# Kernel tuning notes

Hardware: AMD Instinct MI355X
Metric: run time of the kernel (lower is better)

The kernel has to match this reference:

```python
import jax, jax.numpy as jnp
import numpy as np

B, S, H = 4, 2048, 1024
NH, NKV, HD = 16, 4, 64
EPS = 1e-6
SCALE = 1.0 / np.sqrt(HD)
N_REP = NH // NKV


def setup_inputs() -> dict:
    key = jax.random.key(0)
    ks = jax.random.split(key, 8)
    hidden_states = jax.random.normal(ks[0], (B, S, H), dtype=jnp.float32)
    # additive causal mask [1,1,S,S]: 0 on/below diagonal, -1e9 above
    causal_mask = jnp.where(
        jnp.tril(jnp.ones((S, S), dtype=bool)), 0.0, -1e9
    ).astype(jnp.float32)[None, None]
    # interleaved RoPE tables [S, HD] (each frequency repeated twice, matching _rotate_half's even/odd split)
    inv_freq = 1.0 / (10000.0 ** (np.arange(0, HD, 2, dtype=np.float32) / HD))
    angles = jnp.arange(S, dtype=jnp.float32)[:, None] * jnp.asarray(inv_freq)[None, :]
    emb = jnp.repeat(angles, 2, axis=-1)  # [S, HD]
    cos, sin = jnp.cos(emb), jnp.sin(emb)
    # learned params (stored [in, out] for einsum)
    Wq = jax.random.normal(ks[1], (H, NH * HD), dtype=jnp.float32) * 0.02
    Wk = jax.random.normal(ks[2], (H, NKV * HD), dtype=jnp.float32) * 0.02
    Wv = jax.random.normal(ks[3], (H, NKV * HD), dtype=jnp.float32) * 0.02
    Wo = jax.random.normal(ks[4], (NH * HD, H), dtype=jnp.float32) * 0.02
    q_norm_w = jnp.ones((HD,), dtype=jnp.float32)
    k_norm_w = jnp.ones((HD,), dtype=jnp.float32)
    return {"hidden_states": hidden_states, "causal_mask": causal_mask, "cos": cos,
            "sin": sin, "Wq": Wq, "Wk": Wk, "Wv": Wv, "Wo": Wo,
            "q_norm_w": q_norm_w, "k_norm_w": k_norm_w}


def _rms_norm(x, w):
    var = jnp.mean(jnp.square(x), axis=-1, keepdims=True)
    return x * jax.lax.rsqrt(var + EPS) * w


def _rotate_half(x):
    x1 = x[..., ::2]
    x2 = x[..., 1::2]
    return jnp.stack((-x2, x1), axis=-1).reshape(x.shape)


def reference(hidden_states, causal_mask, cos, sin, Wq, Wk, Wv, Wo, q_norm_w, k_norm_w):
    b, s, _ = hidden_states.shape
    q = jnp.einsum('bsh,hd->bsd', hidden_states, Wq).reshape(b, s, NH, HD)
    k = jnp.einsum('bsh,hd->bsd', hidden_states, Wk).reshape(b, s, NKV, HD)
    v = jnp.einsum('bsh,hd->bsd', hidden_states, Wv).reshape(b, s, NKV, HD)
    q = _rms_norm(q, q_norm_w)
    k = _rms_norm(k, k_norm_w)
    q = q.transpose(0, 2, 1, 3)  # [b, NH, s, HD]
    k = k.transpose(0, 2, 1, 3)  # [b, NKV, s, HD]
    v = v.transpose(0, 2, 1, 3)
    c = cos[None, None]  # [1,1,s,HD]
    sn = sin[None, None]
    q = q * c + _rotate_half(q) * sn
    k = k * c + _rotate_half(k) * sn
    if N_REP > 1:
        k = jnp.repeat(k, N_REP, axis=1)  # GQA expand -> [b, NH, s, HD]
        v = jnp.repeat(v, N_REP, axis=1)
    scores = jnp.einsum('bhqd,bhkd->bhqk', q, k) * SCALE + causal_mask
    probs = jax.nn.softmax(scores, axis=-1)
    attn = jnp.einsum('bhqk,bhkd->bhqd', probs, v)
    attn = attn.transpose(0, 2, 1, 3).reshape(b, s, NH * HD)
    return jnp.einsum('bsd,dh->bsh', attn, Wo)
```

## Files before the change

kernel.cpp:

```cpp
#include <hip/hip_runtime.h>

typedef unsigned short u16;
typedef unsigned int u32;

typedef __attribute__((ext_vector_type(8))) short bf16x8;
typedef __attribute__((ext_vector_type(4))) float f32x4;

#define QSCALE 0.18033688011112042f

__device__ __forceinline__ u16 f2bf(float x) {
    union { float f; u32 u; } v; v.f = x;
    u32 r = (v.u + 0x7FFFu + ((v.u >> 16) & 1u)) >> 16;
    return (u16)r;
}
__device__ __forceinline__ float bf2f(u16 x) {
    union { u32 u; float f; } v; v.u = ((u32)x) << 16;
    return v.f;
}
__device__ __forceinline__ u32 pk2(float x, float y) {
    u32 ax = __float_as_uint(x) + 0x8000u;
    u32 ay = __float_as_uint(y) + 0x8000u;
    return __builtin_amdgcn_perm(ay, ax, 0x07060302u);
}

__device__ __forceinline__ void cp16(const u16* g, u16* l) {
    __builtin_amdgcn_global_load_lds(
        (__attribute__((address_space(1))) void*)(g),
        (__attribute__((address_space(3))) void*)(l), 16, 0, 0);
}

__global__ void k_prep(const float* __restrict__ hidden, u16* __restrict__ hA,
                       const float* __restrict__ Wq, u16* __restrict__ WqT,
                       const float* __restrict__ Wk, u16* __restrict__ WkT,
                       const float* __restrict__ Wv, u16* __restrict__ WvT,
                       const float* __restrict__ Wo, u16* __restrict__ WoT) {
    __shared__ u16 t[64][72];
    int bid = blockIdx.x, tid = threadIdx.x;
    if (bid < 4096) {
        int i = (bid * 256 + tid) * 8;
        float4 a = *(const float4*)(hidden + i);
        float4 b = *(const float4*)(hidden + i + 4);
        ushort4 o0; o0.x = f2bf(a.x); o0.y = f2bf(a.y); o0.z = f2bf(a.z); o0.w = f2bf(a.w);
        ushort4 o1; o1.x = f2bf(b.x); o1.y = f2bf(b.y); o1.z = f2bf(b.z); o1.w = f2bf(b.w);
        *(ushort4*)(hA + i) = o0;
        *(ushort4*)(hA + i + 4) = o1;
        return;
    }
    int rb = bid - 4096;
    const float* W; u16* Wt; int N, bx, by;
    if (rb < 256)      { W = Wq; Wt = WqT; N = 1024; bx = rb & 15; by = rb >> 4; }
    else if (rb < 320) { W = Wk; Wt = WkT; N = 256;  rb -= 256; bx = rb & 3; by = rb >> 2; }
    else if (rb < 384) { W = Wv; Wt = WvT; N = 256;  rb -= 320; bx = rb & 3; by = rb >> 2; }
    else               { W = Wo; Wt = WoT; N = 1024; rb -= 384; bx = rb & 15; by = rb >> 4; }
    const int K = 1024;
    int rr = tid >> 2;
    int cs = tid & 3;
    const float* src = W + (by*64 + rr)*N + bx*64 + cs*16;
#pragma unroll
    for (int j = 0; j < 16; j += 4) {
        float4 v = *(const float4*)(src + j);
        t[rr][cs*16 + j + 0] = f2bf(v.x);
        t[rr][cs*16 + j + 1] = f2bf(v.y);
        t[rr][cs*16 + j + 2] = f2bf(v.z);
        t[rr][cs*16 + j + 3] = f2bf(v.w);
    }
    __syncthreads();
    u16* dst = Wt + (bx*64 + rr)*K + by*64 + cs*16;
#pragma unroll
    for (int j = 0; j < 16; ++j) dst[j] = t[cs*16 + j][rr];
}

__device__ __forceinline__ void stage_ab(const u16* __restrict__ Asrc, const u16* __restrict__ Bsrc,
                                         int kt, u16* At, u16* Bt, int tid, int wv) {
#pragma unroll
    for (int i = 0; i < 2; ++i) {
        int q = i*256 + tid;
        int r = q >> 2, sidx = q & 3;
        int s = sidx ^ ((r >> 1) & 3);
        cp16(Asrc + r*1024 + kt*32 + s*8, At + (i*256 + wv*64)*8);
        cp16(Bsrc + r*1024 + kt*32 + s*8, Bt + (i*256 + wv*64)*8);
    }
}

__global__ __launch_bounds__(256) void k_gemm(
    const u16* __restrict__ A,
    const u16* __restrict__ Bq, const u16* __restrict__ Bk, const u16* __restrict__ Bv,
    float* __restrict__ outF,
    u16* __restrict__ outQ, u16* __restrict__ outK, u16* __restrict__ outVT,
    int mode)
{
    __shared__ __align__(16) u16 smem[16384];
    u16* At0 = smem;
    u16* Bt0 = smem + 8192;
    int tid = threadIdx.x;
    int lane = tid & 63, wv = tid >> 6;
    int l15 = lane & 15, quad = lane >> 4;
    int wm = wv >> 1, wn = wv & 1;
    int mb = blockIdx.x, nb = blockIdx.y;

    const u16* Bsrc; int target; int colLocal0;
    if (mode == 0)      { Bsrc = Bq + nb*128*1024;      target = 3; colLocal0 = nb*128; }
    else if (nb < 8)    { Bsrc = Bq + nb*128*1024;      target = 0; colLocal0 = nb*128; }
    else if (nb < 10)   { Bsrc = Bk + (nb-8)*128*1024;  target = 1; colLocal0 = (nb-8)*128; }
    else                { Bsrc = Bv + (nb-10)*128*1024; target = 2; colLocal0 = (nb-10)*128; }
    const u16* Asrc = A + mb*128*1024;

    f32x4 zf = {0.f, 0.f, 0.f, 0.f};
    f32x4 acc[4][4];
#pragma unroll
    for (int i = 0; i < 4; ++i)
#pragma unroll
        for (int j = 0; j < 4; ++j) acc[i][j] = zf;

    stage_ab(Asrc, Bsrc, 0, At0, Bt0, tid, wv);
    __syncthreads();

    for (int kt = 0; kt < 32; ++kt) {
        int cur = kt & 1;
        if (kt < 31) stage_ab(Asrc, Bsrc, kt + 1, At0 + (cur^1)*4096, Bt0 + (cur^1)*4096, tid, wv);
        bf16x8 af[4], bfr[4];
#pragma unroll
        for (int mt = 0; mt < 4; ++mt) {
            int row = wm*64 + mt*16 + l15;
            int sidx = quad ^ ((row >> 1) & 3);
            af[mt] = *(const bf16x8*)(At0 + cur*4096 + row*32 + sidx*8);
        }
#pragma unroll
        for (int nt = 0; nt < 4; ++nt) {
            int row = wn*64 + nt*16 + l15;
            int sidx = quad ^ ((row >> 1) & 3);
            bfr[nt] = *(const bf16x8*)(Bt0 + cur*4096 + row*32 + sidx*8);
        }
#pragma unroll
        for (int mt = 0; mt < 4; ++mt)
#pragma unroll
            for (int nt = 0; nt < 4; ++nt)
                acc[mt][nt] = __builtin_amdgcn_mfma_f32_16x16x32_bf16(af[mt], bfr[nt], acc[mt][nt], 0, 0, 0);
        __syncthreads();
    }

    if (target == 2) {
#pragma unroll
        for (int mt = 0; mt < 4; ++mt) {
#pragma unroll
            for (int nt = 0; nt < 4; ++nt) {
                int cl_local = wn*64 + nt*16 + l15;
                int rowb = wm*64 + mt*16 + quad*4;
                int g = rowb >> 3;
                int sub = (rowb & 7) * 2;
                int gp = g ^ (cl_local & 15);
                uint2 w2;
                w2.x = pk2(acc[mt][nt][0], acc[mt][nt][1]);
                w2.y = pk2(acc[mt][nt][2], acc[mt][nt][3]);
                *(uint2*)((char*)(smem + cl_local*128) + gp*16 + sub) = w2;
            }
        }
        __syncthreads();
        int row0 = mb*128;
        int b = row0 >> 11, s0 = row0 & 2047;
        int dl = tid >> 1, half = tid & 1;
        int cl = colLocal0 + dl;
        int hh = cl >> 6, d = cl & 63;
        u16* dst = outVT + ((b*4 + hh)*64 + d)*2048 + s0 + half*64;
#pragma unroll
        for (int j = 0; j < 8; ++j) {
            int g = half*8 + j;
            int gp = g ^ (dl & 15);
            uint4 vv = *(const uint4*)((const char*)(smem + dl*128) + gp*16);
            *(uint4*)(dst + j*8) = vv;
        }
        return;
    }

#pragma unroll
    for (int mt = 0; mt < 4; ++mt) {
#pragma unroll
        for (int nt = 0; nt < 4; ++nt) {
#pragma unroll
            for (int rr = 0; rr < 4; ++rr) {
                int row = mb*128 + wm*64 + mt*16 + quad*4 + rr;
                int cl  = colLocal0 + wn*64 + nt*16 + l15;
                float v = acc[mt][nt][rr];
                if (target == 3) {
                    outF[row*1024 + cl] = v;
                } else {
                    int b = row >> 11, s = row & 2047;
                    int hh = cl >> 6, d = cl & 63;
                    u16 bv = f2bf(v);
                    if (target == 0)      outQ[((b*16 + hh)*2048 + s)*64 + d] = bv;
                    else                  outK[((b*4  + hh)*2048 + s)*64 + d] = bv;
                }
            }
        }
    }
}

__global__ void k_knorm(u16* __restrict__ K,
                        const float* __restrict__ kw,
                        const float* __restrict__ cosp, const float* __restrict__ sinp)
{
    int row = blockIdx.x * 8 + (threadIdx.x >> 5);
    int tl = threadIdx.x & 31;
    u16* base = K + row*64;
    int s = row & 2047;
    u32 packed = *(const u32*)(base + 2*tl);
    float x0 = bf2f((u16)(packed & 0xffffu));
    float x1 = bf2f((u16)(packed >> 16));
    float ss = x0*x0 + x1*x1;
#pragma unroll
    for (int m = 1; m < 32; m <<= 1) ss += __shfl_xor(ss, m, 32);
    float inv = rsqrtf(ss * (1.0f/64.0f) + 1e-6f);
    float w0 = kw[2*tl], w1 = kw[2*tl+1];
    float c = cosp[s*64 + 2*tl], sn = sinp[s*64 + 2*tl];
    float xn0 = x0 * inv * w0, xn1 = x1 * inv * w1;
    float y0 = xn0*c - xn1*sn;
    float y1 = xn1*c + xn0*sn;
    *(u32*)(base + 2*tl) = pk2(y0, y1);
}

__device__ __forceinline__ void stage_kv(const u16* __restrict__ Kg, const u16* __restrict__ Vg,
                                         int kt, u16* sK, u16* sV, int tid, int wv) {
#pragma unroll
    for (int i = 0; i < 2; ++i) {
        int q = i*256 + tid;
        int r = q >> 3, sidx = q & 7;
        int s = sidx ^ (r & 7);
        cp16(Kg + (kt*64 + r)*64 + s*8, sK + (i*256 + wv*64)*8);
        cp16(Vg + r*2048 + kt*64 + s*8, sV + (i*256 + wv*64)*8);
    }
}

__global__ __launch_bounds__(256, 4) void k_attn(
    const u16* __restrict__ Q, const u16* __restrict__ K,
    const u16* __restrict__ VT, u16* __restrict__ attn,
    const float* __restrict__ qw,
    const float* __restrict__ cosp, const float* __restrict__ sinp)
{
    __shared__ __align__(16) u16 smemP[64*64];
    __shared__ __align__(16) u16 smemK[64*64];
    __shared__ __align__(16) u16 smemV[64*64];

    int tid = threadIdx.x;
    int lane = tid & 63, wv = tid >> 6;
    int l15 = lane & 15, quad = lane >> 4;

    int bid = blockIdx.x;
    int r8 = bid & 7, q8 = bid >> 3;
    int g = ((q8 >> 6) << 3) | r8;
    int local = q8 & 63;
    int b = g >> 2, hkv = g & 3;
    int hl = local >> 4, p = local & 15;
    int h = hkv*4 + hl;

    const u16* Kg = K + ((b*4 + hkv)*2048)*64;
    const u16* Vg = VT + (b*4 + hkv)*64*2048;

    int qcol = wv*16 + l15;

#pragma unroll
    for (int t = 0; t < 2; ++t) {
        int qi = t ? p : (31 - p);
        int q0 = qi * 64;
        const u16* Qg = Q + ((b*16 + h)*2048 + q0)*64;
        int qrow = q0 + qcol;

        bf16x8 qf[2];
        {
            float xv[2][8];
            float ssum = 0.f;
#pragma unroll
            for (int ks = 0; ks < 2; ++ks) {
                bf16x8 raw = *(const bf16x8*)(Qg + qcol*64 + ks*32 + quad*8);
#pragma unroll
                for (int j = 0; j < 8; ++j) {
                    float x = bf2f((u16)raw[j]);
                    xv[ks][j] = x;
                    ssum += x*x;
                }
            }
            ssum += __shfl_xor(ssum, 16);
            ssum += __shfl_xor(ssum, 32);
            float inv = rsqrtf(ssum * (1.0f/64.0f) + 1e-6f);
#pragma unroll
            for (int ks = 0; ks < 2; ++ks) {
                int d0 = ks*32 + quad*8;
                float4 w0 = *(const float4*)(qw + d0);
                float4 w1 = *(const float4*)(qw + d0 + 4);
                float4 c0 = *(const float4*)(cosp + qrow*64 + d0);
                float4 c1 = *(const float4*)(cosp + qrow*64 + d0 + 4);
                float4 s0 = *(const float4*)(sinp + qrow*64 + d0);
                float4 s1 = *(const float4*)(sinp + qrow*64 + d0 + 4);
                float wa[8] = {w0.x,w0.y,w0.z,w0.w,w1.x,w1.y,w1.z,w1.w};
                float ca[8] = {c0.x,c0.y,c0.z,c0.w,c1.x,c1.y,c1.z,c1.w};
                float sa[8] = {s0.x,s0.y,s0.z,s0.w,s1.x,s1.y,s1.z,s1.w};
                union { u32 u[4]; bf16x8 v; } qq;
#pragma unroll
                for (int jj = 0; jj < 4; ++jj) {
                    float xe = xv[ks][2*jj]   * inv * wa[2*jj];
                    float xo = xv[ks][2*jj+1] * inv * wa[2*jj+1];
                    float ye = (xe*ca[2*jj]   - xo*sa[2*jj])   * QSCALE;
                    float yo = (xo*ca[2*jj+1] + xe*sa[2*jj+1]) * QSCALE;
                    qq.u[jj] = pk2(ye, yo);
                }
                qf[ks] = qq.v;
            }
        }

        f32x4 zf = {0.f, 0.f, 0.f, 0.f};
        f32x4 o[4];
#pragma unroll
        for (int mt = 0; mt < 4; ++mt) o[mt] = zf;
        float l_q = 0.f;

        for (int kt = 0; kt <= qi; ++kt) {
            stage_kv(Kg, Vg, kt, smemK, smemV, tid, wv);
            __syncthreads();

            f32x4 sc[4];
#pragma unroll
            for (int mt = 0; mt < 4; ++mt) sc[mt] = zf;
#pragma unroll
            for (int ks = 0; ks < 2; ++ks) {
                bf16x8 kf[4];
#pragma unroll
                for (int mt = 0; mt < 4; ++mt) {
                    int row = mt*16 + l15;
                    int sidx = (ks*4 + quad) ^ (row & 7);
                    kf[mt] = *(const bf16x8*)(smemK + row*64 + sidx*8);
                }
#pragma unroll
                for (int mt = 0; mt < 4; ++mt)
                    sc[mt] = __builtin_amdgcn_mfma_f32_16x16x32_bf16(kf[mt], qf[ks], sc[mt], 0, 0, 0);
            }

            if (kt == qi) {
                int keyb = kt*64 + quad*4;
#pragma unroll
                for (int mt = 0; mt < 4; ++mt)
#pragma unroll
                    for (int rr = 0; rr < 4; ++rr)
                        if (keyb + mt*16 + rr > qrow) sc[mt][rr] = -1e30f;
            }
            float rs = 0.f;
#pragma unroll
            for (int mt = 0; mt < 4; ++mt) {
                float p0 = __builtin_amdgcn_exp2f(sc[mt][0]);
                float p1 = __builtin_amdgcn_exp2f(sc[mt][1]);
                float p2 = __builtin_amdgcn_exp2f(sc[mt][2]);
                float p3 = __builtin_amdgcn_exp2f(sc[mt][3]);
                rs += (p0 + p1) + (p2 + p3);
                uint2 w; w.x = pk2(p0, p1); w.y = pk2(p2, p3);
                int gw = (mt*2 + (quad >> 1)) ^ (qcol & 7);
                *(uint2*)(smemP + qcol*64 + gw*8 + (quad & 1)*4) = w;
            }
            l_q += rs;

#pragma unroll
            for (int ks2 = 0; ks2 < 2; ++ks2) {
                int gr = (ks2*4 + quad) ^ (qcol & 7);
                bf16x8 pf = *(const bf16x8*)(smemP + qcol*64 + gr*8);
                bf16x8 vf[4];
#pragma unroll
                for (int mt = 0; mt < 4; ++mt) {
                    int row = mt*16 + l15;
                    int sidx = (ks2*4 + quad) ^ (row & 7);
                    vf[mt] = *(const bf16x8*)(smemV + row*64 + sidx*8);
                }
#pragma unroll
                for (int mt = 0; mt < 4; ++mt)
                    o[mt] = __builtin_amdgcn_mfma_f32_16x16x32_bf16(vf[mt], pf, o[mt], 0, 0, 0);
            }
            __syncthreads();
        }

        float lt = l_q;
        lt += __shfl_xor(lt, 16);
        lt += __shfl_xor(lt, 32);
        float rl = 1.0f / lt;
#pragma unroll
        for (int mt = 0; mt < 4; ++mt) {
            uint2 w;
            w.x = pk2(o[mt][0]*rl, o[mt][1]*rl);
            w.y = pk2(o[mt][2]*rl, o[mt][3]*rl);
            int gw = (mt*2 + (quad >> 1)) ^ (qcol & 7);
            *(uint2*)(smemP + qcol*64 + gw*8 + (quad & 1)*4) = w;
        }
        __syncthreads();
        {
            int r2 = tid >> 2, c = tid & 3;
            u16* dst = attn + (b*2048 + q0 + r2)*1024 + h*64 + c*16;
            int g0 = (c*2) ^ (r2 & 7);
            int g1 = (c*2 + 1) ^ (r2 & 7);
            *(uint4*)(dst)     = *(const uint4*)(smemP + r2*64 + g0*8);
            *(uint4*)(dst + 8) = *(const uint4*)(smemP + r2*64 + g1*8);
        }
        __syncthreads();
    }
}

extern "C" void kernel_launch(void* const* d_in, const int* in_sizes, int n_in,
                              void* d_out, int out_size, void* d_ws, size_t ws_size,
                              hipStream_t stream) {
    const float* hidden = (const float*)d_in[0];
    const float* cosp = (const float*)d_in[2];
    const float* sinp = (const float*)d_in[3];
    const float* Wq = (const float*)d_in[4];
    const float* Wk = (const float*)d_in[5];
    const float* Wv = (const float*)d_in[6];
    const float* Wo = (const float*)d_in[7];
    const float* qw = (const float*)d_in[8];
    const float* kw = (const float*)d_in[9];
    float* out = (float*)d_out;

    char* ws = (char*)d_ws;
    u16* hA   = (u16*)(ws);
    u16* WqT  = (u16*)(ws + 16777216);
    u16* WkT  = (u16*)(ws + 18874368);
    u16* WvT  = (u16*)(ws + 19398656);
    u16* WoT  = (u16*)(ws + 19922944);
    u16* Qws  = (u16*)(ws + 22020096);
    u16* Kws  = (u16*)(ws + 38797312);
    u16* VTw  = (u16*)(ws + 42991616);
    u16* attn = hA;

    k_prep<<<4736, 256, 0, stream>>>(hidden, hA, Wq, WqT, Wk, WkT, Wv, WvT, Wo, WoT);
    k_gemm<<<dim3(64, 12), 256, 0, stream>>>(hA, WqT, WkT, WvT, nullptr, Qws, Kws, VTw, 1);
    k_knorm<<<4096, 256, 0, stream>>>(Kws, kw, cosp, sinp);
    k_attn<<<1024, 256, 0, stream>>>(Qws, Kws, VTw, attn, qw, cosp, sinp);
    k_gemm<<<dim3(64, 8), 256, 0, stream>>>(attn, WoT, nullptr, nullptr, out, nullptr, nullptr, nullptr, 0);
}
```

Before: 246.8 us.

## Shrink GEMM tiles to 128x64 and split attention to one query tile per block

The GEMM now uses 128x64 tiles with each wave owning 32 rows, which doubles the grid and cuts shared memory. For the V projection it swaps the MFMA operands so each lane writes transposed V directly to global memory instead of staging through LDS. The attention kernel now launches one block per query tile, ordered largest-first, rather than pairing two tiles per block, and issues the first K/V prefetch before the Q norm. The aim is more parallelism and occupancy, at the cost of more redundant A-tile loads and scattered 2-byte VT stores.

```diff
diff --git a/kernel.cpp b/kernel.cpp
--- a/kernel.cpp
+++ b/kernel.cpp
@@ -71,14 +71,18 @@
 }
 
 __device__ __forceinline__ void stage_ab(const u16* __restrict__ Asrc, const u16* __restrict__ Bsrc,
-                                         int kt, u16* At, u16* Bt, int tid, int wv) {
+                                         int kt, u16* buf, int tid, int wv) {
 #pragma unroll
     for (int i = 0; i < 2; ++i) {
         int q = i*256 + tid;
         int r = q >> 2, sidx = q & 3;
         int s = sidx ^ ((r >> 1) & 3);
-        cp16(Asrc + r*1024 + kt*32 + s*8, At + (i*256 + wv*64)*8);
-        cp16(Bsrc + r*1024 + kt*32 + s*8, Bt + (i*256 + wv*64)*8);
+        cp16(Asrc + r*1024 + kt*32 + s*8, buf + i*2048 + wv*512);
+    }
+    {
+        int r = tid >> 2, sidx = tid & 3;
+        int s = sidx ^ ((r >> 1) & 3);
+        cp16(Bsrc + r*1024 + kt*32 + s*8, buf + 4096 + wv*512);
     }
 }
 
@@ -89,106 +93,97 @@
     u16* __restrict__ outQ, u16* __restrict__ outK, u16* __restrict__ outVT,
     int mode)
 {
-    __shared__ __align__(16) u16 smem[16384];
-    u16* At0 = smem;
-    u16* Bt0 = smem + 8192;
+    __shared__ __align__(16) u16 smem[12288];
     int tid = threadIdx.x;
     int lane = tid & 63, wv = tid >> 6;
     int l15 = lane & 15, quad = lane >> 4;
-    int wm = wv >> 1, wn = wv & 1;
     int mb = blockIdx.x, nb = blockIdx.y;
 
-    const u16* Bsrc; int target; int colLocal0;
-    if (mode == 0)      { Bsrc = Bq + nb*128*1024;      target = 3; colLocal0 = nb*128; }
-    else if (nb < 8)    { Bsrc = Bq + nb*128*1024;      target = 0; colLocal0 = nb*128; }
-    else if (nb < 10)   { Bsrc = Bk + (nb-8)*128*1024;  target = 1; colLocal0 = (nb-8)*128; }
-    else                { Bsrc = Bv + (nb-10)*128*1024; target = 2; colLocal0 = (nb-10)*128; }
+    const u16* Bsrc; int target; int hh;
+    if (mode == 0)    { Bsrc = Bq + nb*64*1024;      target = 3; hh = 0; }
+    else if (nb < 16) { Bsrc = Bq + nb*64*1024;      target = 0; hh = nb; }
+    else if (nb < 20) { Bsrc = Bk + (nb-16)*64*1024; target = 1; hh = nb-16; }
+    else              { Bsrc = Bv + (nb-20)*64*1024; target = 2; hh = nb-20; }
     const u16* Asrc = A + mb*128*1024;
+    bool swp = (target == 2);
 
     f32x4 zf = {0.f, 0.f, 0.f, 0.f};
-    f32x4 acc[4][4];
-#pragma unroll
-    for (int i = 0; i < 4; ++i)
+    f32x4 acc[2][4];
+#pragma unroll
+    for (int i = 0; i < 2; ++i)
 #pragma unroll
         for (int j = 0; j < 4; ++j) acc[i][j] = zf;
 
-    stage_ab(Asrc, Bsrc, 0, At0, Bt0, tid, wv);
+    stage_ab(Asrc, Bsrc, 0, smem, tid, wv);
     __syncthreads();
 
     for (int kt = 0; kt < 32; ++kt) {
         int cur = kt & 1;
-        if (kt < 31) stage_ab(Asrc, Bsrc, kt + 1, At0 + (cur^1)*4096, Bt0 + (cur^1)*4096, tid, wv);
-        bf16x8 af[4], bfr[4];
-#pragma unroll
-        for (int mt = 0; mt < 4; ++mt) {
-            int row = wm*64 + mt*16 + l15;
+        if (kt < 31) stage_ab(Asrc, Bsrc, kt + 1, smem + (cur^1)*6144, tid, wv);
+        const u16* buf = smem + cur*6144;
+        bf16x8 af[2], bfr[4];
+#pragma unroll
+        for (int mt = 0; mt < 2; ++mt) {
+            int row = wv*32 + mt*16 + l15;
             int sidx = quad ^ ((row >> 1) & 3);
-            af[mt] = *(const bf16x8*)(At0 + cur*4096 + row*32 + sidx*8);
+            af[mt] = *(const bf16x8*)(buf + row*32 + sidx*8);
         }
 #pragma unroll
         for (int nt = 0; nt < 4; ++nt) {
-            int row = wn*64 + nt*16 + l15;
+            int row = nt*16 + l15;
             int sidx = quad ^ ((row >> 1) & 3);
-            bfr[nt] = *(const bf16x8*)(Bt0 + cur*4096 + row*32 + sidx*8);
-        }
-#pragma unroll
-        for (int mt = 0; mt < 4; ++mt)
-#pragma unroll
-            for (int nt = 0; nt < 4; ++nt)
-                acc[mt][nt] = __builtin_amdgcn_mfma_f32_16x16x32_bf16(af[mt], bfr[nt], acc[mt][nt], 0, 0, 0);
+            bfr[nt] = *(const bf16x8*)(buf + 4096 + row*32 + sidx*8);
+        }
+        if (swp) {
+#pragma unroll
+            for (int mt = 0; mt < 2; ++mt)
+#pragma unroll
+                for (int nt = 0; nt < 4; ++nt)
+                    acc[mt][nt] = __builtin_amdgcn_mfma_f32_16x16x32_bf16(bfr[nt], af[mt], acc[mt][nt], 0, 0, 0);
+        } else {
+#pragma unroll
+            for (int mt = 0; mt < 2; ++mt)
+#pragma unroll
+                for (int nt = 0; nt < 4; ++nt)
+                    acc[mt][nt] = __builtin_amdgcn_mfma_f32_16x16x32_bf16(af[mt], bfr[nt], acc[mt][nt], 0, 0, 0);
+        }
         __syncthreads();
     }
 
     if (target == 2) {
-#pragma unroll
-        for (int mt = 0; mt < 4; ++mt) {
+        int b = mb >> 4, s0 = (mb & 15) * 128;
+#pragma unroll
+        for (int mt = 0; mt < 2; ++mt) {
 #pragma unroll
             for (int nt = 0; nt < 4; ++nt) {
-                int cl_local = wn*64 + nt*16 + l15;
-                int rowb = wm*64 + mt*16 + quad*4;
-                int g = rowb >> 3;
-                int sub = (rowb & 7) * 2;
-                int gp = g ^ (cl_local & 15);
-                uint2 w2;
-                w2.x = pk2(acc[mt][nt][0], acc[mt][nt][1]);
-                w2.y = pk2(acc[mt][nt][2], acc[mt][nt][3]);
-                *(uint2*)((char*)(smem + cl_local*128) + gp*16 + sub) = w2;
-            }
-        }
-        __syncthreads();
-        int row0 = mb*128;
-        int b = row0 >> 11, s0 = row0 & 2047;
-        int dl = tid >> 1, half = tid & 1;
-        int cl = colLocal0 + dl;
-        int hh = cl >> 6, d = cl & 63;
-        u16* dst = outVT + ((b*4 + hh)*64 + d)*2048 + s0 + half*64;
-#pragma unroll
-        for (int j = 0; j < 8; ++j) {
-            int g = half*8 + j;
-            int gp = g ^ (dl & 15);
-            uint4 vv = *(const uint4*)((const char*)(smem + dl*128) + gp*16);
-            *(uint4*)(dst + j*8) = vv;
+#pragma unroll
+                for (int rr = 0; rr < 4; ++rr) {
+                    int s = s0 + wv*32 + mt*16 + l15;
+                    int d = nt*16 + quad*4 + rr;
+                    outVT[((b*4 + hh)*64 + d)*2048 + s] = f2bf(acc[mt][nt][rr]);
+                }
+            }
         }
         return;
     }
 
 #pragma unroll
-    for (int mt = 0; mt < 4; ++mt) {
+    for (int mt = 0; mt < 2; ++mt) {
 #pragma unroll
         for (int nt = 0; nt < 4; ++nt) {
 #pragma unroll
             for (int rr = 0; rr < 4; ++rr) {
-                int row = mb*128 + wm*64 + mt*16 + quad*4 + rr;
-                int cl  = colLocal0 + wn*64 + nt*16 + l15;
+                int row = mb*128 + wv*32 + mt*16 + quad*4 + rr;
                 float v = acc[mt][nt][rr];
                 if (target == 3) {
+                    int cl = nb*64 + nt*16 + l15;
                     outF[row*1024 + cl] = v;
                 } else {
                     int b = row >> 11, s = row & 2047;
-                    int hh = cl >> 6, d = cl & 63;
+                    int d = nt*16 + l15;
                     u16 bv = f2bf(v);
-                    if (target == 0)      outQ[((b*16 + hh)*2048 + s)*64 + d] = bv;
-                    else                  outK[((b*4  + hh)*2048 + s)*64 + d] = bv;
+                    if (target == 0) outQ[((b*16 + hh)*2048 + s)*64 + d] = bv;
+                    else             outK[((b*4  + hh)*2048 + s)*64 + d] = bv;
                 }
             }
         }
@@ -246,155 +241,151 @@
 
     int bid = blockIdx.x;
     int r8 = bid & 7, q8 = bid >> 3;
-    int g = ((q8 >> 6) << 3) | r8;
-    int local = q8 & 63;
+    int g = ((q8 >> 7) << 3) | r8;
+    int local = q8 & 127;
     int b = g >> 2, hkv = g & 3;
-    int hl = local >> 4, p = local & 15;
+    int hl = local >> 5, qi = 31 - (local & 31);
     int h = hkv*4 + hl;
 
     const u16* Kg = K + ((b*4 + hkv)*2048)*64;
     const u16* Vg = VT + (b*4 + hkv)*64*2048;
 
     int qcol = wv*16 + l15;
-
-#pragma unroll
-    for (int t = 0; t < 2; ++t) {
-        int qi = t ? p : (31 - p);
-        int q0 = qi * 64;
-        const u16* Qg = Q + ((b*16 + h)*2048 + q0)*64;
-        int qrow = q0 + qcol;
-
-        bf16x8 qf[2];
-        {
-            float xv[2][8];
-            float ssum = 0.f;
-#pragma unroll
-            for (int ks = 0; ks < 2; ++ks) {
-                bf16x8 raw = *(const bf16x8*)(Qg + qcol*64 + ks*32 + quad*8);
-#pragma unroll
-                for (int j = 0; j < 8; ++j) {
-                    float x = bf2f((u16)raw[j]);
-                    xv[ks][j] = x;
-                    ssum += x*x;
-                }
-            }
-            ssum += __shfl_xor(ssum, 16);
-            ssum += __shfl_xor(ssum, 32);
-            float inv = rsqrtf(ssum * (1.0f/64.0f) + 1e-6f);
-#pragma unroll
-            for (int ks = 0; ks < 2; ++ks) {
-                int d0 = ks*32 + quad*8;
-                float4 w0 = *(const float4*)(qw + d0);
-                float4 w1 = *(const float4*)(qw + d0 + 4);
-                float4 c0 = *(const float4*)(cosp + qrow*64 + d0);
-                float4 c1 = *(const float4*)(cosp + qrow*64 + d0 + 4);
-                float4 s0 = *(const float4*)(sinp + qrow*64 + d0);
-                float4 s1 = *(const float4*)(sinp + qrow*64 + d0 + 4);
-                float wa[8] = {w0.x,w0.y,w0.z,w0.w,w1.x,w1.y,w1.z,w1.w};
-                float ca[8] = {c0.x,c0.y,c0.z,c0.w,c1.x,c1.y,c1.z,c1.w};
-                float sa[8] = {s0.x,s0.y,s0.z,s0.w,s1.x,s1.y,s1.z,s1.w};
-                union { u32 u[4]; bf16x8 v; } qq;
-#pragma unroll
-                for (int jj = 0; jj < 4; ++jj) {
-                    float xe = xv[ks][2*jj]   * inv * wa[2*jj];
-                    float xo = xv[ks][2*jj+1] * inv * wa[2*jj+1];
-                    float ye = (xe*ca[2*jj]   - xo*sa[2*jj])   * QSCALE;
-                    float yo = (xo*ca[2*jj+1] + xe*sa[2*jj+1]) * QSCALE;
-                    qq.u[jj] = pk2(ye, yo);
-                }
-                qf[ks] = qq.v;
-            }
-        }
-
-        f32x4 zf = {0.f, 0.f, 0.f, 0.f};
-        f32x4 o[4];
-#pragma unroll
-        for (int mt = 0; mt < 4; ++mt) o[mt] = zf;
-        float l_q = 0.f;
-
-        for (int kt = 0; kt <= qi; ++kt) {
-            stage_kv(Kg, Vg, kt, smemK, smemV, tid, wv);
-            __syncthreads();
-
-            f32x4 sc[4];
-#pragma unroll
-            for (int mt = 0; mt < 4; ++mt) sc[mt] = zf;
-#pragma unroll
-            for (int ks = 0; ks < 2; ++ks) {
-                bf16x8 kf[4];
-#pragma unroll
-                for (int mt = 0; mt < 4; ++mt) {
-                    int row = mt*16 + l15;
-                    int sidx = (ks*4 + quad) ^ (row & 7);
-                    kf[mt] = *(const bf16x8*)(smemK + row*64 + sidx*8);
-                }
-#pragma unroll
-                for (int mt = 0; mt < 4; ++mt)
-                    sc[mt] = __builtin_amdgcn_mfma_f32_16x16x32_bf16(kf[mt], qf[ks], sc[mt], 0, 0, 0);
-            }
-
-            if (kt == qi) {
-                int keyb = kt*64 + quad*4;
-#pragma unroll
-                for (int mt = 0; mt < 4; ++mt)
-#pragma unroll
-                    for (int rr = 0; rr < 4; ++rr)
-                        if (keyb + mt*16 + rr > qrow) sc[mt][rr] = -1e30f;
-            }
-            float rs = 0.f;
+    int q0 = qi * 64;
+    const u16* Qg = Q + ((b*16 + h)*2048 + q0)*64;
+    int qrow = q0 + qcol;
+
+    stage_kv(Kg, Vg, 0, smemK, smemV, tid, wv);
+
+    bf16x8 qf[2];
+    {
+        float xv[2][8];
+        float ssum = 0.f;
+#pragma unroll
+        for (int ks = 0; ks < 2; ++ks) {
+            bf16x8 raw = *(const bf16x8*)(Qg + qcol*64 + ks*32 + quad*8);
+#pragma unroll
+            for (int j = 0; j < 8; ++j) {
+                float x = bf2f((u16)raw[j]);
+                xv[ks][j] = x;
+                ssum += x*x;
+            }
+        }
+        ssum += __shfl_xor(ssum, 16);
+        ssum += __shfl_xor(ssum, 32);
+        float inv = rsqrtf(ssum * (1.0f/64.0f) + 1e-6f);
+#pragma unroll
+        for (int ks = 0; ks < 2; ++ks) {
+            int d0 = ks*32 + quad*8;
+            float4 w0 = *(const float4*)(qw + d0);
+            float4 w1 = *(const float4*)(qw + d0 + 4);
+            float4 c0 = *(const float4*)(cosp + qrow*64 + d0);
+            float4 c1 = *(const float4*)(cosp + qrow*64 + d0 + 4);
+            float4 s0 = *(const float4*)(sinp + qrow*64 + d0);
+            float4 s1 = *(const float4*)(sinp + qrow*64 + d0 + 4);
+            float wa[8] = {w0.x,w0.y,w0.z,w0.w,w1.x,w1.y,w1.z,w1.w};
+            float ca[8] = {c0.x,c0.y,c0.z,c0.w,c1.x,c1.y,c1.z,c1.w};
+            float sa[8] = {s0.x,s0.y,s0.z,s0.w,s1.x,s1.y,s1.z,s1.w};
+            union { u32 u[4]; bf16x8 v; } qq;
+#pragma unroll
+            for (int jj = 0; jj < 4; ++jj) {
+                float xe = xv[ks][2*jj]   * inv * wa[2*jj];
+                float xo = xv[ks][2*jj+1] * inv * wa[2*jj+1];
+                float ye = (xe*ca[2*jj]   - xo*sa[2*jj])   * QSCALE;
+                float yo = (xo*ca[2*jj+1] + xe*sa[2*jj+1]) * QSCALE;
+                qq.u[jj] = pk2(ye, yo);
+            }
+            qf[ks] = qq.v;
+        }
+    }
+
+    f32x4 zf = {0.f, 0.f, 0.f, 0.f};
+    f32x4 o[4];
+#pragma unroll
+    for (int mt = 0; mt < 4; ++mt) o[mt] = zf;
+    float l_q = 0.f;
+
+    for (int kt = 0; kt <= qi; ++kt) {
+        if (kt > 0) stage_kv(Kg, Vg, kt, smemK, smemV, tid, wv);
+        __syncthreads();
+
+        f32x4 sc[4];
+#pragma unroll
+        for (int mt = 0; mt < 4; ++mt) sc[mt] = zf;
+#pragma unroll
+        for (int ks = 0; ks < 2; ++ks) {
+            bf16x8 kf[4];
 #pragma unroll
             for (int mt = 0; mt < 4; ++mt) {
-                float p0 = __builtin_amdgcn_exp2f(sc[mt][0]);
-                float p1 = __builtin_amdgcn_exp2f(sc[mt][1]);
-                float p2 = __builtin_amdgcn_exp2f(sc[mt][2]);
-                float p3 = __builtin_amdgcn_exp2f(sc[mt][3]);
-                rs += (p0 + p1) + (p2 + p3);
-                uint2 w; w.x = pk2(p0, p1); w.y = pk2(p2, p3);
-                int gw = (mt*2 + (quad >> 1)) ^ (qcol & 7);
-                *(uint2*)(smemP + qcol*64 + gw*8 + (quad & 1)*4) = w;
-            }
-            l_q += rs;
-
-#pragma unroll
-            for (int ks2 = 0; ks2 < 2; ++ks2) {
-                int gr = (ks2*4 + quad) ^ (qcol & 7);
-                bf16x8 pf = *(const bf16x8*)(smemP + qcol*64 + gr*8);
-                bf16x8 vf[4];
-#pragma unroll
-                for (int mt = 0; mt < 4; ++mt) {
-                    int row = mt*16 + l15;
-                    int sidx = (ks2*4 + quad) ^ (row & 7);
-                    vf[mt] = *(const bf16x8*)(smemV + row*64 + sidx*8);
-                }
-#pragma unroll
-                for (int mt = 0; mt < 4; ++mt)
-                    o[mt] = __builtin_amdgcn_mfma_f32_16x16x32_bf16(vf[mt], pf, o[mt], 0, 0, 0);
-            }
-            __syncthreads();
-        }
-
-        float lt = l_q;
-        lt += __shfl_xor(lt, 16);
-        lt += __shfl_xor(lt, 32);
-        float rl = 1.0f / lt;
+                int row = mt*16 + l15;
+                int sidx = (ks*4 + quad) ^ (row & 7);
+                kf[mt] = *(const bf16x8*)(smemK + row*64 + sidx*8);
+            }
+#pragma unroll
+            for (int mt = 0; mt < 4; ++mt)
+                sc[mt] = __builtin_amdgcn_mfma_f32_16x16x32_bf16(kf[mt], qf[ks], sc[mt], 0, 0, 0);
+        }
+
+        if (kt == qi) {
+            int keyb = kt*64 + quad*4;
+#pragma unroll
+            for (int mt = 0; mt < 4; ++mt)
+#pragma unroll
+                for (int rr = 0; rr < 4; ++rr)
+                    if (keyb + mt*16 + rr > qrow) sc[mt][rr] = -1e30f;
+        }
+        float rs = 0.f;
 #pragma unroll
         for (int mt = 0; mt < 4; ++mt) {
-            uint2 w;
-            w.x = pk2(o[mt][0]*rl, o[mt][1]*rl);
-            w.y = pk2(o[mt][2]*rl, o[mt][3]*rl);
+            float p0 = __builtin_amdgcn_exp2f(sc[mt][0]);
+            float p1 = __builtin_amdgcn_exp2f(sc[mt][1]);
+            float p2 = __builtin_amdgcn_exp2f(sc[mt][2]);
+            float p3 = __builtin_amdgcn_exp2f(sc[mt][3]);
+            rs += (p0 + p1) + (p2 + p3);
+            uint2 w; w.x = pk2(p0, p1); w.y = pk2(p2, p3);
             int gw = (mt*2 + (quad >> 1)) ^ (qcol & 7);
             *(uint2*)(smemP + qcol*64 + gw*8 + (quad & 1)*4) = w;
         }
+        l_q += rs;
+
+#pragma unroll
+        for (int ks2 = 0; ks2 < 2; ++ks2) {
+            int gr = (ks2*4 + quad) ^ (qcol & 7);
+            bf16x8 pf = *(const bf16x8*)(smemP + qcol*64 + gr*8);
+            bf16x8 vf[4];
+#pragma unroll
+            for (int mt = 0; mt < 4; ++mt) {
+                int row = mt*16 + l15;
+                int sidx = (ks2*4 + quad) ^ (row & 7);
+                vf[mt] = *(const bf16x8*)(smemV + row*64 + sidx*8);
+            }
+#pragma unroll
+            for (int mt = 0; mt < 4; ++mt)
+                o[mt] = __builtin_amdgcn_mfma_f32_16x16x32_bf16(vf[mt], pf, o[mt], 0, 0, 0);
+        }
         __syncthreads();
-        {
-            int r2 = tid >> 2, c = tid & 3;
-            u16* dst = attn + (b*2048 + q0 + r2)*1024 + h*64 + c*16;
-            int g0 = (c*2) ^ (r2 & 7);
-            int g1 = (c*2 + 1) ^ (r2 & 7);
-            *(uint4*)(dst)     = *(const uint4*)(smemP + r2*64 + g0*8);
-            *(uint4*)(dst + 8) = *(const uint4*)(smemP + r2*64 + g1*8);
-        }
-        __syncthreads();
+    }
+
+    float lt = l_q;
+    lt += __shfl_xor(lt, 16);
+    lt += __shfl_xor(lt, 32);
+    float rl = 1.0f / lt;
+#pragma unroll
+    for (int mt = 0; mt < 4; ++mt) {
+        uint2 w;
+        w.x = pk2(o[mt][0]*rl, o[mt][1]*rl);
+        w.y = pk2(o[mt][2]*rl, o[mt][3]*rl);
+        int gw = (mt*2 + (quad >> 1)) ^ (qcol & 7);
+        *(uint2*)(smemP + qcol*64 + gw*8 + (quad & 1)*4) = w;
+    }
+    __syncthreads();
+    {
+        int r2 = tid >> 2, c = tid & 3;
+        u16* dst = attn + (b*2048 + q0 + r2)*1024 + h*64 + c*16;
+        int g0 = (c*2) ^ (r2 & 7);
+        int g1 = (c*2 + 1) ^ (r2 & 7);
+        *(uint4*)(dst)     = *(const uint4*)(smemP + r2*64 + g0*8);
+        *(uint4*)(dst + 8) = *(const uint4*)(smemP + r2*64 + g1*8);
     }
 }
 
@@ -424,8 +415,8 @@
     u16* attn = hA;
 
     k_prep<<<4736, 256, 0, stream>>>(hidden, hA, Wq, WqT, Wk, WkT, Wv, WvT, Wo, WoT);
-    k_gemm<<<dim3(64, 12), 256, 0, stream>>>(hA, WqT, WkT, WvT, nullptr, Qws, Kws, VTw, 1);
+    k_gemm<<<dim3(64, 24), 256, 0, stream>>>(hA, WqT, WkT, WvT, nullptr, Qws, Kws, VTw, 1);
     k_knorm<<<4096, 256, 0, stream>>>(Kws, kw, cosp, sinp);
-    k_attn<<<1024, 256, 0, stream>>>(Qws, Kws, VTw, attn, qw, cosp, sinp);
-    k_gemm<<<dim3(64, 8), 256, 0, stream>>>(attn, WoT, nullptr, nullptr, out, nullptr, nullptr, nullptr, 0);
-}
+    k_attn<<<2048, 256, 0, stream>>>(Qws, Kws, VTw, attn, qw, cosp, sinp);
+    k_gemm<<<dim3(64, 16), 256, 0, stream>>>(attn, WoT, nullptr, nullptr, out, nullptr, nullptr, nullptr, 0);
+}
```

Result: no change. 251.6 us (+1.9%).
